# Kernel optimization log

Hardware: AMD Instinct MI355X
Metric: run time of the kernel (lower is better)

The kernel has to match this reference:

```python
import jax, jax.numpy as jnp
import numpy as np

DIM = 1024
HEADS = 8
HEAD_DIM = DIM // HEADS
TAU = HEAD_DIM ** 0.5
BS, SEQ = 1, 2048


def setup_inputs() -> dict:
    key = jax.random.key(0)
    kq, kk, kv, kb = jax.random.split(key, 4)
    q = jax.random.normal(kq, (BS, SEQ, DIM), jnp.float32)
    k = jax.random.normal(kk, (BS, SEQ, DIM), jnp.float32)
    v = jax.random.normal(kv, (BS, SEQ, DIM), jnp.float32)
    Wi_w = jnp.zeros((HEADS, 3 * DIM), jnp.float32)
    Wi_b = 0.1 * jax.random.normal(kb, (HEADS,), jnp.float32)
    Wf_w = jnp.zeros((HEADS, 3 * DIM), jnp.float32)
    Wf_b = jnp.linspace(3.0, 6.0, HEADS, dtype=jnp.float32)  # equidistant_bias_init(3, 6)
    gn_w = jnp.ones((DIM,), jnp.float32)
    gn_b = jnp.zeros((DIM,), jnp.float32)
    return {"q": q, "k": k, "v": v, "Wi_w": Wi_w, "Wi_b": Wi_b,
            "Wf_w": Wf_w, "Wf_b": Wf_b, "gn_w": gn_w, "gn_b": gn_b}


def reference(q, k, v, Wi_w, Wi_b, Wf_w, Wf_b, gn_w, gn_b):
    bs, seq, dim = q.shape
    gate_in = jnp.concatenate([q, k, v], axis=-1)                    # [b, s, 3d]
    itilde = jnp.einsum('bsd,hd->bhs', gate_in, Wi_w) + Wi_b[None, :, None]
    ftilde = jnp.einsum('bsd,hd->bhs', gate_in, Wf_w) + Wf_b[None, :, None]

    # Decay matrix: F_act[i,j] = sum_{t=j+1..i} logsigmoid(ftilde_t), lower-tri else -inf
    csum = jnp.cumsum(jax.nn.log_sigmoid(ftilde), axis=-1)           # [b, h, s]
    Fmat = csum[..., :, None] - csum[..., None, :]                   # [b, h, s, s]
    mask = jnp.tril(jnp.ones((seq, seq), dtype=bool))
    F_act = jnp.where(mask, Fmat, -jnp.inf)

    Dtilde = F_act + itilde[..., None, :]                            # add input gate along j
    max_d = jnp.max(Dtilde, axis=-1, keepdims=True)
    D = jnp.exp(Dtilde - max_d)                                      # stabilized decay weights

    qh = q.reshape(bs, seq, HEADS, HEAD_DIM).transpose(0, 2, 1, 3)
    kh = k.reshape(bs, seq, HEADS, HEAD_DIM).transpose(0, 2, 1, 3)
    vh = v.reshape(bs, seq, HEADS, HEAD_DIM).transpose(0, 2, 1, 3)

    Ctilde = jnp.einsum('bhid,bhjd->bhij', qh, kh) * D / TAU
    maxit = jnp.maximum(jnp.abs(jnp.sum(Ctilde, axis=-1, keepdims=True)), jnp.exp(-max_d))
    Htilde = jnp.einsum('bhij,bhjd->bhid', Ctilde, vh) / (maxit + 1e-6)

    # GroupNorm(HEADS groups) over dim, applied per token
    x = Htilde.transpose(0, 2, 1, 3).reshape(bs * seq, HEADS, HEAD_DIM)
    mean = jnp.mean(x, axis=-1, keepdims=True)
    var = jnp.var(x, axis=-1, keepdims=True)
    xn = (x - mean) / jnp.sqrt(var + 1e-5)
    out = xn.reshape(bs * seq, DIM) * gn_w + gn_b
    return out.reshape(bs, seq, DIM)
```

## Files before the change

kernel.cpp:

```cpp
#include <hip/hip_runtime.h>
#include <math.h>

#define SEQ 2048
#define NH 8
#define HD 128
#define DIMF 1024
#define LOG2E 1.4426950408889634f
#define INVTAU 0.08838834764831845f

typedef __attribute__((ext_vector_type(8))) short bf16x8;
typedef __attribute__((ext_vector_type(8))) unsigned short us8;
typedef __attribute__((ext_vector_type(4))) float f32x4;

__device__ float g_itacc[NH*SEQ];
__device__ float g_ftacc[NH*SEQ];
__device__ float g_aL[NH*SEQ];
__device__ float g_cmL[NH*SEQ];
__device__ float g_en[NH*SEQ];
__device__ unsigned short g_Qb[NH*SEQ*HD];
__device__ unsigned short g_Kb[NH*SEQ*HD];
__device__ unsigned short g_Vb[NH*SEQ*HD];
__device__ unsigned short g_Vt[NH*HD*SEQ];
__device__ unsigned short g_Wb[16*3072];
__device__ float g_Opart[640*64*128];
__device__ float g_Spart[640*64];

__device__ __forceinline__ unsigned short f2bf(float x) {
  unsigned u = __float_as_uint(x);
  u += 0x7fffu + ((u >> 16) & 1u);
  return (unsigned short)(u >> 16);
}

__global__ __launch_bounds__(256) void convert_kernel(const float* __restrict__ q,
                                                      const float* __restrict__ k,
                                                      const float* __restrict__ Wi,
                                                      const float* __restrict__ Wf) {
  const int bid = blockIdx.x;
  if (bid < 4096) {
    const int s = bid & 2047;
    const int t = bid >> 11;
    const float* src = (t == 0) ? q : k;
    unsigned short* dst = (t == 0) ? g_Qb : g_Kb;
    const int c = threadIdx.x * 4;
    const float4 f = *(const float4*)(src + s*DIMF + c);
    const int h = c >> 7, d = c & 127;
    ushort4 u;
    u.x = f2bf(f.x); u.y = f2bf(f.y); u.z = f2bf(f.z); u.w = f2bf(f.w);
    *(ushort4*)(dst + (h*SEQ + s)*HD + d) = u;
  } else {
    const int gid = (bid - 4096) * 256 + threadIdx.x;
    const int e4 = gid * 4;
    const int p = e4 / 3072;
    const int c = e4 % 3072;
    const float* src = (p < 8) ? (Wi + p*3072 + c) : (Wf + (p-8)*3072 + c);
    const float4 f = *(const float4*)src;
    ushort4 u;
    u.x = f2bf(f.x); u.y = f2bf(f.y); u.z = f2bf(f.z); u.w = f2bf(f.w);
    *(ushort4*)(g_Wb + p*3072 + c) = u;
  }
}

__global__ __launch_bounds__(256) void vtrans_kernel(const float* __restrict__ v) {
  __shared__ __align__(16) unsigned short Ts[64*72];
  const int h  = blockIdx.x;
  const int s0 = blockIdx.y * 64;
  const int d0 = blockIdx.z * 64;
  const int t = threadIdx.x;
  {
    const int sr = t >> 2;
    const int c  = (t & 3) * 16;
    const float* src = v + (s0 + sr)*DIMF + h*HD + d0 + c;
    unsigned short tmp[16];
    #pragma unroll
    for (int i = 0; i < 4; ++i) {
      const float4 f = *(const float4*)&src[i*4];
      tmp[i*4+0] = f2bf(f.x); tmp[i*4+1] = f2bf(f.y);
      tmp[i*4+2] = f2bf(f.z); tmp[i*4+3] = f2bf(f.w);
    }
    *(us8*)&Ts[sr*72 + c]     = *(us8*)&tmp[0];
    *(us8*)&Ts[sr*72 + c + 8] = *(us8*)&tmp[8];
    unsigned short* vb = g_Vb + (h*SEQ + s0 + sr)*HD + d0 + c;
    *(us8*)&vb[0] = *(us8*)&tmp[0];
    *(us8*)&vb[8] = *(us8*)&tmp[8];
  }
  __syncthreads();
  {
    const int w = t >> 6, l = t & 63;
    unsigned short outv[16];
    #pragma unroll
    for (int j = 0; j < 16; ++j) outv[j] = Ts[(w*16 + j)*72 + l];
    unsigned short* dst = g_Vt + (h*HD + d0 + l)*SEQ + s0 + w*16;
    *(us8*)&dst[0] = *(us8*)&outv[0];
    *(us8*)&dst[8] = *(us8*)&outv[8];
  }
}

__global__ __launch_bounds__(256) void gates_kernel() {
  __shared__ f32x4 red[4][64];
  const int tid = threadIdx.x;
  const int wave = tid >> 6, lane = tid & 63;
  const int q4 = lane >> 4, l16 = lane & 15;
  const int s0 = blockIdx.x * 16;
  f32x4 acc = {0.f, 0.f, 0.f, 0.f};
  #pragma unroll 8
  for (int ks = wave*24; ks < wave*24 + 24; ++ks) {
    const int k0 = ks*32 + q4*8;
    const int tsel = k0 >> 10;
    const int rem = k0 & 1023;
    const int hh = rem >> 7, dd = rem & 127;
    const unsigned short* base = (tsel == 0) ? g_Qb : (tsel == 1) ? g_Kb : g_Vb;
    const bf16x8 a = *(const bf16x8*)&base[(hh*SEQ + s0 + l16)*HD + dd];
    const bf16x8 b = *(const bf16x8*)&g_Wb[l16*3072 + k0];
    acc = __builtin_amdgcn_mfma_f32_16x16x32_bf16(a, b, acc, 0, 0, 0);
  }
  red[wave][lane] = acc;
  __syncthreads();
  if (wave == 0) {
    f32x4 s = red[0][lane];
    #pragma unroll
    for (int w = 1; w < 4; ++w) s += red[w][lane];
    #pragma unroll
    for (int r = 0; r < 4; ++r) {
      const int sg = s0 + 4*q4 + r;
      if (l16 < 8) g_itacc[l16*SEQ + sg] = s[r];
      else         g_ftacc[(l16-8)*SEQ + sg] = s[r];
    }
  }
}

__global__ __launch_bounds__(256) void scan_kernel(const float* __restrict__ Wi_b,
                                                   const float* __restrict__ Wf_b) {
  __shared__ float Wsum[4];
  __shared__ float Wmax[4];
  const int h = blockIdx.x;
  const int t = threadIdx.x;
  const int wave = t >> 6, lane = t & 63;
  const float ib = Wi_b[h];
  const float fb = Wf_b[h];
  const int base = h*SEQ + t*8;

  float it[8], ft[8];
  *(float4*)&it[0] = *(const float4*)&g_itacc[base];
  *(float4*)&it[4] = *(const float4*)&g_itacc[base+4];
  *(float4*)&ft[0] = *(const float4*)&g_ftacc[base];
  *(float4*)&ft[4] = *(const float4*)&g_ftacc[base+4];

  float cs[8];
  float run = 0.f;
  #pragma unroll
  for (int j = 0; j < 8; ++j) {
    const float f = ft[j] + fb;
    const float ls = fminf(f, 0.f) - log1pf(expf(-fabsf(f)));
    run += ls;
    cs[j] = run;
  }
  float x = run;
  #pragma unroll
  for (int off = 1; off < 64; off <<= 1) {
    const float tv = __shfl_up(x, off, 64);
    if (lane >= off) x += tv;
  }
  const float wexcl = x - run;
  if (lane == 63) Wsum[wave] = x;
  __syncthreads();
  float boff = 0.f;
  #pragma unroll
  for (int w = 0; w < 4; ++w) if (w < wave) boff += Wsum[w];
  const float cbase = boff + wexcl;

  float a[8], am[8], csum[8];
  float m = -__builtin_inff();
  #pragma unroll
  for (int j = 0; j < 8; ++j) {
    csum[j] = cbase + cs[j];
    a[j] = (it[j] + ib) - csum[j];
    m = fmaxf(m, a[j]);
    am[j] = m;
  }
  float y = m;
  #pragma unroll
  for (int off = 1; off < 64; off <<= 1) {
    const float tv = __shfl_up(y, off, 64);
    if (lane >= off) y = fmaxf(y, tv);
  }
  float e = __shfl_up(y, 1, 64);
  if (lane == 0) e = -__builtin_inff();
  if (lane == 63) Wmax[wave] = y;
  __syncthreads();
  float bmax = -__builtin_inff();
  #pragma unroll
  for (int w = 0; w < 4; ++w) if (w < wave) bmax = fmaxf(bmax, Wmax[w]);
  const float pre = fmaxf(bmax, e);

  float oa[8], ocm[8], oen[8];
  #pragma unroll
  for (int j = 0; j < 8; ++j) {
    const float cm = fmaxf(pre, am[j]);
    oa[j]  = a[j] * LOG2E;
    ocm[j] = cm * LOG2E;
    oen[j] = expf(-(csum[j] + cm));
  }
  *(float4*)&g_aL[base]    = *(float4*)&oa[0];
  *(float4*)&g_aL[base+4]  = *(float4*)&oa[4];
  *(float4*)&g_cmL[base]   = *(float4*)&ocm[0];
  *(float4*)&g_cmL[base+4] = *(float4*)&ocm[4];
  *(float4*)&g_en[base]    = *(float4*)&oen[0];
  *(float4*)&g_en[base+4]  = *(float4*)&oen[4];
}

__global__ __launch_bounds__(256, 3) void attn1_kernel() {
  __shared__ __align__(16) unsigned short Ps[2][64*72];
  __shared__ float Sred[64][2];

  const int h = blockIdx.x;
  const int y = blockIdx.y;
  int g, s0g;
  if      (y < 8)  { g = 0; s0g = 0;  }
  else if (y < 24) { g = 1; s0g = 8;  }
  else if (y < 48) { g = 2; s0g = 24; }
  else             { g = 3; s0g = 48; }
  const int rel = y - s0g;
  const int iT  = 8*g + rel/(g+1);
  const int ch  = rel - (rel/(g+1))*(g+1);
  const int slot = h*80 + y;
  const int i0 = iT*64;
  const int jt0 = ch*8;
  const int jt1 = (jt0 + 8 < iT + 1) ? (jt0 + 8) : (iT + 1);

  const int tid = threadIdx.x;
  const int wave = tid >> 6;
  const int lane = tid & 63;
  const int q4 = lane >> 4;
  const int l16 = lane & 15;
  const int wr = wave >> 1;
  const int wc = wave & 1;

  bf16x8 qa[2][4];
  {
    const unsigned short* Qg = g_Qb + (h*SEQ + i0 + 32*wr + l16)*HD;
    #pragma unroll
    for (int tr = 0; tr < 2; ++tr)
      #pragma unroll
      for (int ks = 0; ks < 4; ++ks)
        qa[tr][ks] = *(const bf16x8*)&Qg[tr*16*HD + ks*32 + q4*8];
  }

  float cmv[2][4];
  #pragma unroll
  for (int tr = 0; tr < 2; ++tr)
    #pragma unroll
    for (int r = 0; r < 4; ++r)
      cmv[tr][r] = g_cmL[h*SEQ + i0 + 32*wr + 16*tr + 4*q4 + r];

  f32x4 accH[2][4];
  float rs[2][4];
  const f32x4 fzero = {0.f, 0.f, 0.f, 0.f};
  #pragma unroll
  for (int tr = 0; tr < 2; ++tr) {
    #pragma unroll
    for (int tc = 0; tc < 4; ++tc) accH[tr][tc] = fzero;
    #pragma unroll
    for (int r = 0; r < 4; ++r) rs[tr][r] = 0.f;
  }

  const unsigned short* Kgh = g_Kb + (h*SEQ)*HD;
  const unsigned short* Vgh = g_Vt + (h*HD)*SEQ;

  for (int jt = jt0; jt < jt1; ++jt) {
    const int j0 = jt*64;
    const int b = (jt - jt0) & 1;
    unsigned short* Pb = &Ps[b][0];

    float aLv[2];
    aLv[0] = g_aL[h*SEQ + j0 + 32*wc + l16];
    aLv[1] = g_aL[h*SEQ + j0 + 32*wc + 16 + l16];

    f32x4 c00 = fzero, c01 = fzero, c10 = fzero, c11 = fzero;
    #pragma unroll
    for (int ks = 0; ks < 4; ++ks) {
      const int ko = ks*32 + q4*8;
      const bf16x8 b0 = *(const bf16x8*)&Kgh[(j0 + 32*wc      + l16)*HD + ko];
      const bf16x8 b1 = *(const bf16x8*)&Kgh[(j0 + 32*wc + 16 + l16)*HD + ko];
      c00 = __builtin_amdgcn_mfma_f32_16x16x32_bf16(qa[0][ks], b0, c00, 0, 0, 0);
      c01 = __builtin_amdgcn_mfma_f32_16x16x32_bf16(qa[0][ks], b1, c01, 0, 0, 0);
      c10 = __builtin_amdgcn_mfma_f32_16x16x32_bf16(qa[1][ks], b0, c10, 0, 0, 0);
      c11 = __builtin_amdgcn_mfma_f32_16x16x32_bf16(qa[1][ks], b1, c11, 0, 0, 0);
    }

    const bool diag = (jt == iT);
    #pragma unroll
    for (int tr = 0; tr < 2; ++tr) {
      #pragma unroll
      for (int tc = 0; tc < 2; ++tc) {
        const f32x4 cc = tr ? (tc ? c11 : c10) : (tc ? c01 : c00);
        const int jg = j0 + 32*wc + 16*tc + l16;
        #pragma unroll
        for (int r = 0; r < 4; ++r) {
          const int rloc = 32*wr + 16*tr + 4*q4 + r;
          const int ig = i0 + rloc;
          const float w = exp2f(aLv[tc] - cmv[tr][r]) * INVTAU;
          float p = cc[r] * w;
          if (diag && (jg > ig)) p = 0.f;
          rs[tr][r] += p;
          Pb[rloc*72 + 32*wc + 16*tc + l16] = f2bf(p);
        }
      }
    }
    __syncthreads();

    #pragma unroll
    for (int ks = 0; ks < 2; ++ks) {
      const int ko = ks*32 + q4*8;
      const bf16x8 p0 = *(const bf16x8*)&Pb[(32*wr      + l16)*72 + ko];
      const bf16x8 p1 = *(const bf16x8*)&Pb[(32*wr + 16 + l16)*72 + ko];
      #pragma unroll
      for (int tc = 0; tc < 4; ++tc) {
        const bf16x8 vb = *(const bf16x8*)&Vgh[(64*wc + 16*tc + l16)*SEQ + j0 + ko];
        accH[0][tc] = __builtin_amdgcn_mfma_f32_16x16x32_bf16(p0, vb, accH[0][tc], 0, 0, 0);
        accH[1][tc] = __builtin_amdgcn_mfma_f32_16x16x32_bf16(p1, vb, accH[1][tc], 0, 0, 0);
      }
    }
  }

  #pragma unroll
  for (int tr = 0; tr < 2; ++tr)
    #pragma unroll
    for (int r = 0; r < 4; ++r) {
      float t = rs[tr][r];
      t += __shfl_xor(t, 1, 16);
      t += __shfl_xor(t, 2, 16);
      t += __shfl_xor(t, 4, 16);
      t += __shfl_xor(t, 8, 16);
      rs[tr][r] = t;
    }
  if (l16 == 0) {
    #pragma unroll
    for (int tr = 0; tr < 2; ++tr)
      #pragma unroll
      for (int r = 0; r < 4; ++r)
        Sred[32*wr + 16*tr + 4*q4 + r][wc] = rs[tr][r];
  }
  __syncthreads();

  if (tid < 64) g_Spart[slot*64 + tid] = Sred[tid][0] + Sred[tid][1];

  float* Ob = g_Opart + slot*(64*128);
  #pragma unroll
  for (int tr = 0; tr < 2; ++tr)
    #pragma unroll
    for (int r = 0; r < 4; ++r) {
      const int rloc = 32*wr + 16*tr + 4*q4 + r;
      #pragma unroll
      for (int tc = 0; tc < 4; ++tc)
        Ob[rloc*128 + 64*wc + 16*tc + l16] = accH[tr][tc][r];
    }
}

__global__ __launch_bounds__(256) void reduce_kernel(const float* __restrict__ gnw,
                                                     const float* __restrict__ gnb,
                                                     float* __restrict__ out) {
  const int h  = blockIdx.x;
  const int iT = blockIdx.y;
  const int t  = threadIdx.x;
  const int r  = t >> 2;
  const int qd = t & 3;
  const int qq = iT >> 3;
  const int nch = qq + 1;
  const int slot0 = h*80 + iT + 4*qq*(qq-1) + qq*(iT & 7);

  float acc[32];
  #pragma unroll
  for (int e = 0; e < 32; ++e) acc[e] = 0.f;
  float S = 0.f;
  for (int c = 0; c < nch; ++c) {
    const float* Ob = g_Opart + (slot0 + c)*(64*128) + r*128 + qd*32;
    #pragma unroll
    for (int kk = 0; kk < 8; ++kk) {
      const float4 f = *(const float4*)&Ob[kk*4];
      acc[kk*4+0] += f.x; acc[kk*4+1] += f.y; acc[kk*4+2] += f.z; acc[kk*4+3] += f.w;
    }
    S += g_Spart[(slot0 + c)*64 + r];
  }

  const float en = g_en[h*SEQ + iT*64 + r];
  const float sc = 1.f / (fmaxf(fabsf(S), en) + 1e-6f);
  float s1 = 0.f, s2 = 0.f;
  #pragma unroll
  for (int e = 0; e < 32; ++e) {
    const float xv = acc[e] * sc;
    acc[e] = xv;
    s1 += xv;
    s2 += xv * xv;
  }
  s1 += __shfl_xor(s1, 1, 4); s2 += __shfl_xor(s2, 1, 4);
  s1 += __shfl_xor(s1, 2, 4); s2 += __shfl_xor(s2, 2, 4);
  const float mean = s1 * (1.f/128.f);
  const float var  = s2 * (1.f/128.f) - mean*mean;
  const float rstd = rsqrtf(var + 1e-5f);

  const float* gw = gnw + h*HD + qd*32;
  const float* gb = gnb + h*HD + qd*32;
  float* op = out + (iT*64 + r)*DIMF + h*HD + qd*32;
  #pragma unroll
  for (int kk = 0; kk < 8; ++kk) {
    const float4 w4 = *(const float4*)&gw[kk*4];
    const float4 b4 = *(const float4*)&gb[kk*4];
    float4 o;
    o.x = (acc[kk*4+0] - mean) * rstd * w4.x + b4.x;
    o.y = (acc[kk*4+1] - mean) * rstd * w4.y + b4.y;
    o.z = (acc[kk*4+2] - mean) * rstd * w4.z + b4.z;
    o.w = (acc[kk*4+3] - mean) * rstd * w4.w + b4.w;
    *(float4*)&op[kk*4] = o;
  }
}

extern "C" void kernel_launch(void* const* d_in, const int* in_sizes, int n_in,
                              void* d_out, int out_size, void* d_ws, size_t ws_size,
                              hipStream_t stream) {
  (void)in_sizes; (void)n_in; (void)out_size; (void)d_ws; (void)ws_size;
  const float* q    = (const float*)d_in[0];
  const float* k    = (const float*)d_in[1];
  const float* v    = (const float*)d_in[2];
  const float* Wi_w = (const float*)d_in[3];
  const float* Wi_b = (const float*)d_in[4];
  const float* Wf_w = (const float*)d_in[5];
  const float* Wf_b = (const float*)d_in[6];
  const float* gnw  = (const float*)d_in[7];
  const float* gnb  = (const float*)d_in[8];
  float* out = (float*)d_out;

  convert_kernel<<<dim3(4144), 256, 0, stream>>>(q, k, Wi_w, Wf_w);
  vtrans_kernel<<<dim3(NH, SEQ/64, HD/64), 256, 0, stream>>>(v);
  gates_kernel<<<dim3(128), 256, 0, stream>>>();
  scan_kernel<<<dim3(NH), 256, 0, stream>>>(Wi_b, Wf_b);
  attn1_kernel<<<dim3(NH, 80), 256, 0, stream>>>();
  reduce_kernel<<<dim3(NH, SEQ/64), 256, 0, stream>>>(gnw, gnb, out);
}
```

Measured before the change: 166.6 us.

## Restructure attention to per-wave row tiles, fold tau scale, merge prep kernels

Each wave in the attention kernel now owns 16 query rows across the full 64-key and 128-dim tile. P stays in a wave-private LDS slice, so block-wide barriers and the cross-wave row-sum reduction are gone. The 1/tau scale is folded into the exponent as a -3.5 offset in log2 space, since log2(1/sqrt(128)) is exactly -3.5, which removes one multiply per element. The bf16 convert and V-transpose kernels are merged into a single launch. The trade-off is that each wave now loads all K and V fragments itself, which raises global/L2 traffic and register pressure.

After: 207.9 us. +24.8%, slower.

```diff
diff --git a/kernel.cpp b/kernel.cpp
--- a/kernel.cpp
+++ b/kernel.cpp
@@ -6,7 +6,6 @@
 #define HD 128
 #define DIMF 1024
 #define LOG2E 1.4426950408889634f
-#define INVTAU 0.08838834764831845f
 
 typedef __attribute__((ext_vector_type(8))) short bf16x8;
 typedef __attribute__((ext_vector_type(8))) unsigned short us8;
@@ -31,10 +30,12 @@
   return (unsigned short)(u >> 16);
 }
 
-__global__ __launch_bounds__(256) void convert_kernel(const float* __restrict__ q,
-                                                      const float* __restrict__ k,
-                                                      const float* __restrict__ Wi,
-                                                      const float* __restrict__ Wf) {
+__global__ __launch_bounds__(256) void prep_kernel(const float* __restrict__ q,
+                                                   const float* __restrict__ k,
+                                                   const float* __restrict__ v,
+                                                   const float* __restrict__ Wi,
+                                                   const float* __restrict__ Wf) {
+  __shared__ __align__(16) unsigned short Ts[64*72];
   const int bid = blockIdx.x;
   if (bid < 4096) {
     const int s = bid & 2047;
@@ -47,7 +48,7 @@
     ushort4 u;
     u.x = f2bf(f.x); u.y = f2bf(f.y); u.z = f2bf(f.z); u.w = f2bf(f.w);
     *(ushort4*)(dst + (h*SEQ + s)*HD + d) = u;
-  } else {
+  } else if (bid < 4144) {
     const int gid = (bid - 4096) * 256 + threadIdx.x;
     const int e4 = gid * 4;
     const int p = e4 / 3072;
@@ -57,41 +58,39 @@
     ushort4 u;
     u.x = f2bf(f.x); u.y = f2bf(f.y); u.z = f2bf(f.z); u.w = f2bf(f.w);
     *(ushort4*)(g_Wb + p*3072 + c) = u;
-  }
-}
-
-__global__ __launch_bounds__(256) void vtrans_kernel(const float* __restrict__ v) {
-  __shared__ __align__(16) unsigned short Ts[64*72];
-  const int h  = blockIdx.x;
-  const int s0 = blockIdx.y * 64;
-  const int d0 = blockIdx.z * 64;
-  const int t = threadIdx.x;
-  {
-    const int sr = t >> 2;
-    const int c  = (t & 3) * 16;
-    const float* src = v + (s0 + sr)*DIMF + h*HD + d0 + c;
-    unsigned short tmp[16];
-    #pragma unroll
-    for (int i = 0; i < 4; ++i) {
-      const float4 f = *(const float4*)&src[i*4];
-      tmp[i*4+0] = f2bf(f.x); tmp[i*4+1] = f2bf(f.y);
-      tmp[i*4+2] = f2bf(f.z); tmp[i*4+3] = f2bf(f.w);
-    }
-    *(us8*)&Ts[sr*72 + c]     = *(us8*)&tmp[0];
-    *(us8*)&Ts[sr*72 + c + 8] = *(us8*)&tmp[8];
-    unsigned short* vb = g_Vb + (h*SEQ + s0 + sr)*HD + d0 + c;
-    *(us8*)&vb[0] = *(us8*)&tmp[0];
-    *(us8*)&vb[8] = *(us8*)&tmp[8];
-  }
-  __syncthreads();
-  {
-    const int w = t >> 6, l = t & 63;
-    unsigned short outv[16];
-    #pragma unroll
-    for (int j = 0; j < 16; ++j) outv[j] = Ts[(w*16 + j)*72 + l];
-    unsigned short* dst = g_Vt + (h*HD + d0 + l)*SEQ + s0 + w*16;
-    *(us8*)&dst[0] = *(us8*)&outv[0];
-    *(us8*)&dst[8] = *(us8*)&outv[8];
+  } else {
+    const int b2 = bid - 4144;
+    const int h  = b2 & 7;
+    const int s0 = ((b2 >> 3) & 31) * 64;
+    const int d0 = (b2 >> 8) * 64;
+    const int t = threadIdx.x;
+    {
+      const int sr = t >> 2;
+      const int c  = (t & 3) * 16;
+      const float* src = v + (s0 + sr)*DIMF + h*HD + d0 + c;
+      unsigned short tmp[16];
+      #pragma unroll
+      for (int i = 0; i < 4; ++i) {
+        const float4 f = *(const float4*)&src[i*4];
+        tmp[i*4+0] = f2bf(f.x); tmp[i*4+1] = f2bf(f.y);
+        tmp[i*4+2] = f2bf(f.z); tmp[i*4+3] = f2bf(f.w);
+      }
+      *(us8*)&Ts[sr*72 + c]     = *(us8*)&tmp[0];
+      *(us8*)&Ts[sr*72 + c + 8] = *(us8*)&tmp[8];
+      unsigned short* vb = g_Vb + (h*SEQ + s0 + sr)*HD + d0 + c;
+      *(us8*)&vb[0] = *(us8*)&tmp[0];
+      *(us8*)&vb[8] = *(us8*)&tmp[8];
+    }
+    __syncthreads();
+    {
+      const int w = t >> 6, l = t & 63;
+      unsigned short outv[16];
+      #pragma unroll
+      for (int j = 0; j < 16; ++j) outv[j] = Ts[(w*16 + j)*72 + l];
+      unsigned short* dst = g_Vt + (h*HD + d0 + l)*SEQ + s0 + w*16;
+      *(us8*)&dst[0] = *(us8*)&outv[0];
+      *(us8*)&dst[8] = *(us8*)&outv[8];
+    }
   }
 }
 
@@ -196,7 +195,7 @@
   #pragma unroll
   for (int j = 0; j < 8; ++j) {
     const float cm = fmaxf(pre, am[j]);
-    oa[j]  = a[j] * LOG2E;
+    oa[j]  = a[j] * LOG2E - 3.5f;
     ocm[j] = cm * LOG2E;
     oen[j] = expf(-(csum[j] + cm));
   }
@@ -209,8 +208,7 @@
 }
 
 __global__ __launch_bounds__(256, 3) void attn1_kernel() {
-  __shared__ __align__(16) unsigned short Ps[2][64*72];
-  __shared__ float Sred[64][2];
+  __shared__ __align__(16) unsigned short Pl[4][16*72];
 
   const int h = blockIdx.x;
   const int y = blockIdx.y;
@@ -232,128 +230,105 @@
   const int lane = tid & 63;
   const int q4 = lane >> 4;
   const int l16 = lane & 15;
-  const int wr = wave >> 1;
-  const int wc = wave & 1;
-
-  bf16x8 qa[2][4];
+  const int ir0 = i0 + 16*wave;
+  unsigned short* Pw = &Pl[wave][0];
+
+  bf16x8 qa[4];
   {
-    const unsigned short* Qg = g_Qb + (h*SEQ + i0 + 32*wr + l16)*HD;
-    #pragma unroll
-    for (int tr = 0; tr < 2; ++tr)
-      #pragma unroll
-      for (int ks = 0; ks < 4; ++ks)
-        qa[tr][ks] = *(const bf16x8*)&Qg[tr*16*HD + ks*32 + q4*8];
-  }
-
-  float cmv[2][4];
-  #pragma unroll
-  for (int tr = 0; tr < 2; ++tr)
-    #pragma unroll
-    for (int r = 0; r < 4; ++r)
-      cmv[tr][r] = g_cmL[h*SEQ + i0 + 32*wr + 16*tr + 4*q4 + r];
-
-  f32x4 accH[2][4];
-  float rs[2][4];
+    const unsigned short* Qg = g_Qb + (h*SEQ + ir0 + l16)*HD;
+    #pragma unroll
+    for (int ks = 0; ks < 4; ++ks) qa[ks] = *(const bf16x8*)&Qg[ks*32 + q4*8];
+  }
+
+  float cmv[4];
+  #pragma unroll
+  for (int r = 0; r < 4; ++r) cmv[r] = g_cmL[h*SEQ + ir0 + 4*q4 + r];
+
+  f32x4 acc[8];
+  float rs[4];
   const f32x4 fzero = {0.f, 0.f, 0.f, 0.f};
   #pragma unroll
-  for (int tr = 0; tr < 2; ++tr) {
-    #pragma unroll
-    for (int tc = 0; tc < 4; ++tc) accH[tr][tc] = fzero;
-    #pragma unroll
-    for (int r = 0; r < 4; ++r) rs[tr][r] = 0.f;
-  }
-
-  const unsigned short* Kgh = g_Kb + (h*SEQ)*HD;
-  const unsigned short* Vgh = g_Vt + (h*HD)*SEQ;
+  for (int tc = 0; tc < 8; ++tc) acc[tc] = fzero;
+  #pragma unroll
+  for (int r = 0; r < 4; ++r) rs[r] = 0.f;
+
+  const unsigned short* Kgh = g_Kb + h*SEQ*HD;
+  const unsigned short* Vgh = g_Vt + h*HD*SEQ;
+  const float* aLg = g_aL + h*SEQ;
 
   for (int jt = jt0; jt < jt1; ++jt) {
     const int j0 = jt*64;
-    const int b = (jt - jt0) & 1;
-    unsigned short* Pb = &Ps[b][0];
-
-    float aLv[2];
-    aLv[0] = g_aL[h*SEQ + j0 + 32*wc + l16];
-    aLv[1] = g_aL[h*SEQ + j0 + 32*wc + 16 + l16];
-
-    f32x4 c00 = fzero, c01 = fzero, c10 = fzero, c11 = fzero;
-    #pragma unroll
-    for (int ks = 0; ks < 4; ++ks) {
-      const int ko = ks*32 + q4*8;
-      const bf16x8 b0 = *(const bf16x8*)&Kgh[(j0 + 32*wc      + l16)*HD + ko];
-      const bf16x8 b1 = *(const bf16x8*)&Kgh[(j0 + 32*wc + 16 + l16)*HD + ko];
-      c00 = __builtin_amdgcn_mfma_f32_16x16x32_bf16(qa[0][ks], b0, c00, 0, 0, 0);
-      c01 = __builtin_amdgcn_mfma_f32_16x16x32_bf16(qa[0][ks], b1, c01, 0, 0, 0);
-      c10 = __builtin_amdgcn_mfma_f32_16x16x32_bf16(qa[1][ks], b0, c10, 0, 0, 0);
-      c11 = __builtin_amdgcn_mfma_f32_16x16x32_bf16(qa[1][ks], b1, c11, 0, 0, 0);
-    }
+
+    float aLv[4];
+    #pragma unroll
+    for (int jc = 0; jc < 4; ++jc) aLv[jc] = aLg[j0 + jc*16 + l16];
+
+    bf16x8 kf[16];
+    #pragma unroll
+    for (int jc = 0; jc < 4; ++jc)
+      #pragma unroll
+      for (int ks = 0; ks < 4; ++ks)
+        kf[jc*4+ks] = *(const bf16x8*)&Kgh[(j0 + jc*16 + l16)*HD + ks*32 + q4*8];
+
+    f32x4 c[4] = {fzero, fzero, fzero, fzero};
+    #pragma unroll
+    for (int ks = 0; ks < 4; ++ks)
+      #pragma unroll
+      for (int jc = 0; jc < 4; ++jc)
+        c[jc] = __builtin_amdgcn_mfma_f32_16x16x32_bf16(qa[ks], kf[jc*4+ks], c[jc], 0, 0, 0);
+
+    bf16x8 vf[16];
+    #pragma unroll
+    for (int tc = 0; tc < 8; ++tc)
+      #pragma unroll
+      for (int ks = 0; ks < 2; ++ks)
+        vf[tc*2+ks] = *(const bf16x8*)&Vgh[(tc*16 + l16)*SEQ + j0 + ks*32 + q4*8];
 
     const bool diag = (jt == iT);
     #pragma unroll
-    for (int tr = 0; tr < 2; ++tr) {
-      #pragma unroll
-      for (int tc = 0; tc < 2; ++tc) {
-        const f32x4 cc = tr ? (tc ? c11 : c10) : (tc ? c01 : c00);
-        const int jg = j0 + 32*wc + 16*tc + l16;
-        #pragma unroll
-        for (int r = 0; r < 4; ++r) {
-          const int rloc = 32*wr + 16*tr + 4*q4 + r;
-          const int ig = i0 + rloc;
-          const float w = exp2f(aLv[tc] - cmv[tr][r]) * INVTAU;
-          float p = cc[r] * w;
-          if (diag && (jg > ig)) p = 0.f;
-          rs[tr][r] += p;
-          Pb[rloc*72 + 32*wc + 16*tc + l16] = f2bf(p);
-        }
+    for (int jc = 0; jc < 4; ++jc) {
+      const int jg = j0 + jc*16 + l16;
+      #pragma unroll
+      for (int r = 0; r < 4; ++r) {
+        const int ig = ir0 + 4*q4 + r;
+        float p = c[jc][r] * exp2f(aLv[jc] - cmv[r]);
+        if (diag && (jg > ig)) p = 0.f;
+        rs[r] += p;
+        Pw[(4*q4 + r)*72 + jc*16 + l16] = f2bf(p);
       }
     }
-    __syncthreads();
-
-    #pragma unroll
-    for (int ks = 0; ks < 2; ++ks) {
-      const int ko = ks*32 + q4*8;
-      const bf16x8 p0 = *(const bf16x8*)&Pb[(32*wr      + l16)*72 + ko];
-      const bf16x8 p1 = *(const bf16x8*)&Pb[(32*wr + 16 + l16)*72 + ko];
-      #pragma unroll
-      for (int tc = 0; tc < 4; ++tc) {
-        const bf16x8 vb = *(const bf16x8*)&Vgh[(64*wc + 16*tc + l16)*SEQ + j0 + ko];
-        accH[0][tc] = __builtin_amdgcn_mfma_f32_16x16x32_bf16(p0, vb, accH[0][tc], 0, 0, 0);
-        accH[1][tc] = __builtin_amdgcn_mfma_f32_16x16x32_bf16(p1, vb, accH[1][tc], 0, 0, 0);
-      }
-    }
-  }
-
-  #pragma unroll
-  for (int tr = 0; tr < 2; ++tr)
-    #pragma unroll
-    for (int r = 0; r < 4; ++r) {
-      float t = rs[tr][r];
-      t += __shfl_xor(t, 1, 16);
-      t += __shfl_xor(t, 2, 16);
-      t += __shfl_xor(t, 4, 16);
-      t += __shfl_xor(t, 8, 16);
-      rs[tr][r] = t;
-    }
+
+    const bf16x8 pf0 = *(const bf16x8*)&Pw[l16*72 + q4*8];
+    const bf16x8 pf1 = *(const bf16x8*)&Pw[l16*72 + 32 + q4*8];
+
+    #pragma unroll
+    for (int tc = 0; tc < 8; ++tc) {
+      acc[tc] = __builtin_amdgcn_mfma_f32_16x16x32_bf16(pf0, vf[tc*2+0], acc[tc], 0, 0, 0);
+      acc[tc] = __builtin_amdgcn_mfma_f32_16x16x32_bf16(pf1, vf[tc*2+1], acc[tc], 0, 0, 0);
+    }
+  }
+
+  #pragma unroll
+  for (int r = 0; r < 4; ++r) {
+    float t = rs[r];
+    t += __shfl_xor(t, 1, 16);
+    t += __shfl_xor(t, 2, 16);
+    t += __shfl_xor(t, 4, 16);
+    t += __shfl_xor(t, 8, 16);
+    rs[r] = t;
+  }
   if (l16 == 0) {
     #pragma unroll
-    for (int tr = 0; tr < 2; ++tr)
-      #pragma unroll
-      for (int r = 0; r < 4; ++r)
-        Sred[32*wr + 16*tr + 4*q4 + r][wc] = rs[tr][r];
-  }
-  __syncthreads();
-
-  if (tid < 64) g_Spart[slot*64 + tid] = Sred[tid][0] + Sred[tid][1];
+    for (int r = 0; r < 4; ++r)
+      g_Spart[slot*64 + 16*wave + 4*q4 + r] = rs[r];
+  }
 
   float* Ob = g_Opart + slot*(64*128);
   #pragma unroll
-  for (int tr = 0; tr < 2; ++tr)
-    #pragma unroll
-    for (int r = 0; r < 4; ++r) {
-      const int rloc = 32*wr + 16*tr + 4*q4 + r;
-      #pragma unroll
-      for (int tc = 0; tc < 4; ++tc)
-        Ob[rloc*128 + 64*wc + 16*tc + l16] = accH[tr][tc][r];
-    }
+  for (int tc = 0; tc < 8; ++tc)
+    #pragma unroll
+    for (int r = 0; r < 4; ++r)
+      Ob[(16*wave + 4*q4 + r)*128 + tc*16 + l16] = acc[tc][r];
 }
 
 __global__ __launch_bounds__(256) void reduce_kernel(const float* __restrict__ gnw,
@@ -429,8 +404,7 @@
   const float* gnb  = (const float*)d_in[8];
   float* out = (float*)d_out;
 
-  convert_kernel<<<dim3(4144), 256, 0, stream>>>(q, k, Wi_w, Wf_w);
-  vtrans_kernel<<<dim3(NH, SEQ/64, HD/64), 256, 0, stream>>>(v);
+  prep_kernel<<<dim3(4656), 256, 0, stream>>>(q, k, v, Wi_w, Wf_w);
   gates_kernel<<<dim3(128), 256, 0, stream>>>();
   scan_kernel<<<dim3(NH), 256, 0, stream>>>(Wi_b, Wf_b);
   attn1_kernel<<<dim3(NH, 80), 256, 0, stream>>>();
```
